# Optimization experiments

Measured on AMD Instinct MI355X. Metric: run time of the kernel, lower is better.

The kernel has to match this reference:

```python
import jax, jax.numpy as jnp
import numpy as np

B, S = 2, 1024
HIDDEN = 2048
NUM_K, NUM_V = 16, 32
DK, DV = 128, 128
KCONV = 4
EPS = 1e-6
KEY_DIM = NUM_K * DK      # 2048
VAL_DIM = NUM_V * DV      # 4096
RATIO = NUM_V // NUM_K    # 2


def setup_inputs() -> dict:
    key = jax.random.key(0)
    ks = jax.random.split(key, 8)
    sc = lambda k, shape, s=0.02: jax.random.normal(k, shape, jnp.float32) * s
    return {
        "hidden_states": jax.random.normal(ks[0], (B, S, HIDDEN), jnp.float32),
        "W_qkvz": sc(ks[1], (HIDDEN, 2 * KEY_DIM + 2 * VAL_DIM)),
        "W_ba": sc(ks[2], (HIDDEN, 2 * NUM_V)),
        "conv_weight": sc(ks[3], (2 * KEY_DIM + VAL_DIM, KCONV), 0.1),
        "A_log": jnp.log(jax.random.uniform(ks[4], (NUM_V,), jnp.float32, 0.001, 16.0)),
        "dt_bias": jnp.ones((NUM_V,), jnp.float32),
        "norm_weight": jnp.ones((DV,), jnp.float32),
        "W_out": sc(ks[5], (VAL_DIM, HIDDEN)),
    }


def _l2norm(x):
    return x * jax.lax.rsqrt(jnp.sum(x * x, axis=-1, keepdims=True) + 1e-6)


def reference(hidden_states, W_qkvz, W_ba, conv_weight, A_log, dt_bias, norm_weight, W_out):
    Bb, Ss, _ = hidden_states.shape
    # fused in_proj + fix_query_key_value_ordering: per k-head layout [q|k|ratio*v|ratio*z]
    qkvz = (hidden_states @ W_qkvz).reshape(Bb, Ss, NUM_K, 2 * DK + 2 * RATIO * DV)
    q = qkvz[..., :DK]                                        # [B,S,NUM_K,DK]
    k = qkvz[..., DK:2 * DK]
    v = qkvz[..., 2 * DK:2 * DK + RATIO * DV].reshape(Bb, Ss, NUM_V, DV)
    z = qkvz[..., 2 * DK + RATIO * DV:].reshape(Bb, Ss, NUM_V, DV)
    ba = (hidden_states @ W_ba).reshape(Bb, Ss, NUM_K, 2 * RATIO)
    b = ba[..., :RATIO].reshape(Bb, Ss, NUM_V)
    a = ba[..., RATIO:].reshape(Bb, Ss, NUM_V)
    # causal depthwise conv over mixed qkv channels + silu (causal_conv1d)
    mixed = jnp.concatenate(
        [q.reshape(Bb, Ss, -1), k.reshape(Bb, Ss, -1), v.reshape(Bb, Ss, -1)], axis=-1)
    x = jnp.transpose(mixed, (0, 2, 1))                       # [B,C,S]
    x = jnp.pad(x, ((0, 0), (0, 0), (KCONV - 1, 0)))
    conv = jax.lax.conv_general_dilated(
        x, conv_weight[:, None, :], (1,), 'VALID',
        feature_group_count=x.shape[1],
        dimension_numbers=('NCH', 'OIH', 'NCH'))
    mixed = jax.nn.silu(jnp.transpose(conv, (0, 2, 1)))       # [B,S,conv_dim]
    q = mixed[..., :KEY_DIM].reshape(Bb, Ss, NUM_K, DK)
    k = mixed[..., KEY_DIM:2 * KEY_DIM].reshape(Bb, Ss, NUM_K, DK)
    v = mixed[..., 2 * KEY_DIM:].reshape(Bb, Ss, NUM_V, DV)
    # GQA: repeat each k-head to its RATIO consecutive v-heads
    q = jnp.repeat(q, RATIO, axis=2)
    k = jnp.repeat(k, RATIO, axis=2)
    q = _l2norm(q) * (DK ** -0.5)
    k = _l2norm(k)
    # fused_gdn_gating: g = -exp(A_log) * softplus(a + dt_bias); beta = sigmoid(b)
    g = -jnp.exp(A_log) * jax.nn.softplus(a + dt_bias)        # [B,S,H] fp32
    beta = jax.nn.sigmoid(b)
    # recurrent gated delta rule scan; state [B,H,DK,DV]
    def step(state, inp):
        qt, kt, vt, gt, bt = inp
        state = state * jnp.exp(gt)[..., None, None]
        pred = jnp.einsum('bhk,bhkv->bhv', kt, state)
        delta = (vt - pred) * bt[..., None]
        state = state + kt[..., None] * delta[..., None, :]
        out = jnp.einsum('bhk,bhkv->bhv', qt, state)
        return state, out

    xs = (q.transpose(1, 0, 2, 3), k.transpose(1, 0, 2, 3), v.transpose(1, 0, 2, 3),
          g.transpose(1, 0, 2), beta.transpose(1, 0, 2))
    state0 = jnp.zeros((Bb, NUM_V, DK, DV), jnp.float32)
    _, core = jax.lax.scan(step, state0, xs)                  # [S,B,H,DV]
    core = core.transpose(1, 0, 2, 3)
    # RMSNormGated (norm_before_gate=True): rmsnorm(x) * w * silu(z)
    var = jnp.mean(core * core, axis=-1, keepdims=True)
    core = core * jax.lax.rsqrt(var + EPS) * norm_weight * jax.nn.silu(z)
    return core.reshape(Bb, Ss, VAL_DIM) @ W_out              # [B,S,HIDDEN]
```

## Files before the change

### kernel.cpp

```cpp
#include <hip/hip_runtime.h>
#include <stdint.h>

#define B_ 2
#define S_ 1024
#define HID 2048
#define NK 16
#define NV 32
#define DK_ 128
#define DV_ 128
#define QKVZ_N 12288
#define TOK (B_*S_)

typedef unsigned short u16;
typedef __bf16 bf16x8 __attribute__((ext_vector_type(8)));
typedef float f32x4 __attribute__((ext_vector_type(4)));
typedef unsigned short u16x8 __attribute__((ext_vector_type(8)));
typedef unsigned short u16x4 __attribute__((ext_vector_type(4)));

__device__ __forceinline__ float bf2f(u16 u) {
    return __builtin_bit_cast(float, (unsigned)u << 16);
}
__device__ __forceinline__ u16 f2bf(float f) {
    unsigned u = __builtin_bit_cast(unsigned, f);
    u += 0x7fff + ((u >> 16) & 1);
    return (u16)(u >> 16);
}

__device__ __forceinline__ void gl16(const void* g, void* l) {
    __builtin_amdgcn_global_load_lds((const __attribute__((address_space(1))) uint32_t*)g,
                                     (__attribute__((address_space(3))) uint32_t*)l, 16, 0, 0);
}

__device__ __forceinline__ bf16x8 fragld(const u16* base, int row, int col, int rowhw) {
    int idx = row * rowhw + ((((col >> 3) ^ (row & 7))) << 3);
    return __builtin_bit_cast(bf16x8, *(const u16x8*)(base + idx));
}
__device__ __forceinline__ int swzidx(int row, int col, int rowhw) {
    return row * rowhw + (((col >> 3) ^ (row & 7)) << 3) + (col & 7);
}

__global__ void k_cvt_bf16(const float* __restrict__ in, u16* __restrict__ out, int n) {
    int i = (blockIdx.x * blockDim.x + threadIdx.x) * 4;
    if (i >= n) return;
    float4 v = *(const float4*)(in + i);
    u16x4 o = { f2bf(v.x), f2bf(v.y), f2bf(v.z), f2bf(v.w) };
    *(u16x4*)(out + i) = o;
}

__global__ void k_transpose(const float* __restrict__ in, u16* __restrict__ out, int R, int C) {
    __shared__ float tile[32][33];
    int c0 = blockIdx.x * 32, r0 = blockIdx.y * 32;
    int tx = threadIdx.x, ty = threadIdx.y;
#pragma unroll
    for (int i = 0; i < 4; i++)
        tile[ty + i * 8][tx] = in[(size_t)(r0 + ty + i * 8) * C + c0 + tx];
    __syncthreads();
#pragma unroll
    for (int i = 0; i < 4; i++)
        out[(size_t)(c0 + ty + i * 8) * R + r0 + tx] = f2bf(tile[tx][ty + i * 8]);
}

template <int OUT_BF16>
__global__ __launch_bounds__(256) void k_gemm(const u16* __restrict__ A, const u16* __restrict__ Bt,
                                              void* __restrict__ Cv, int K, int ldc) {
    __shared__ u16 As[128 * 32];
    __shared__ u16 Bs[128 * 32];
    int tid = threadIdx.x;
    int bm = blockIdx.y, bn = blockIdx.x;
    int wid = tid >> 6, lane = tid & 63;
    int wm = wid >> 1, wn = wid & 1;
    int l15 = lane & 15, lg = lane >> 4;
    const u16* src0 = (wid >> 1) ? (Bt + (size_t)bn * 128 * K) : (A + (size_t)bm * 128 * K);
    u16* ldsb = (wid >> 1) ? Bs : As;
    int cbase = (wid & 1) * 4;
    int lrow = lane >> 2, lcol = (lane & 3) * 8;
    f32x4 acc[4][4] = {};
    for (int k0 = 0; k0 < K; k0 += 32) {
        if (k0) __syncthreads();
#pragma unroll
        for (int c = 0; c < 4; c++) {
            int ch = cbase + c;
            gl16(src0 + (size_t)(16 * ch + lrow) * K + k0 + lcol, (char*)ldsb + ch * 1024);
        }
        __syncthreads();
        bf16x8 af[4], bf[4];
#pragma unroll
        for (int mi = 0; mi < 4; mi++)
            af[mi] = __builtin_bit_cast(bf16x8, *(const u16x8*)&As[(wm * 64 + mi * 16 + l15) * 32 + lg * 8]);
#pragma unroll
        for (int ni = 0; ni < 4; ni++)
            bf[ni] = __builtin_bit_cast(bf16x8, *(const u16x8*)&Bs[(wn * 64 + ni * 16 + l15) * 32 + lg * 8]);
#pragma unroll
        for (int mi = 0; mi < 4; mi++)
#pragma unroll
            for (int ni = 0; ni < 4; ni++)
                acc[mi][ni] = __builtin_amdgcn_mfma_f32_16x16x32_bf16(af[mi], bf[ni], acc[mi][ni], 0, 0, 0);
    }
#pragma unroll
    for (int mi = 0; mi < 4; mi++) {
        int gr0 = bm * 128 + wm * 64 + mi * 16 + lg * 4;
#pragma unroll
        for (int ni = 0; ni < 4; ni++) {
            int gc = bn * 128 + wn * 64 + ni * 16 + l15;
#pragma unroll
            for (int r = 0; r < 4; r++) {
                if (OUT_BF16)
                    ((u16*)Cv)[(size_t)(gr0 + r) * ldc + gc] = f2bf(acc[mi][ni][r]);
                else
                    ((float*)Cv)[(size_t)(gr0 + r) * ldc + gc] = acc[mi][ni][r];
            }
        }
    }
}

__global__ void k_ba(const float* __restrict__ hid, const float* __restrict__ Wba, float* __restrict__ ba) {
    int token = blockIdx.x;
    int c = threadIdx.x;
    const float* h = hid + (size_t)token * HID;
    const float* w = Wba + c;
    float acc = 0.f;
    for (int k = 0; k < HID; k += 4) {
        float4 hv = *(const float4*)(h + k);
        acc += hv.x * w[(size_t)k * 64] + hv.y * w[(size_t)(k + 1) * 64] +
               hv.z * w[(size_t)(k + 2) * 64] + hv.w * w[(size_t)(k + 3) * 64];
    }
    ba[(size_t)token * 64 + c] = acc;
}

__global__ __launch_bounds__(256) void k_conv(const u16* __restrict__ qkvz, const float* __restrict__ ba,
                                              const float* __restrict__ cw, const float* __restrict__ A_log,
                                              const float* __restrict__ dt_bias, u16* __restrict__ qsb,
                                              u16* __restrict__ ksb, u16* __restrict__ vsb,
                                              float2* __restrict__ gb2) {
    __shared__ float sm[4096];
    int token = blockIdx.x;
    int b = token >> 10;
    int t = token & (S_ - 1);
    int tid = threadIdx.x;
    const u16* row3 = qkvz + (size_t)token * QKVZ_N;
#pragma unroll
    for (int i = 0; i < 32; i++) {
        int c = tid + i * 256;
        int col;
        if (c < 2048) col = (c >> 7) * 768 + (c & 127);
        else if (c < 4096) col = ((c - 2048) >> 7) * 768 + 128 + (c & 127);
        else {
            int cc = c - 4096;
            col = (cc >> 8) * 768 + 256 + ((cc >> 7) & 1) * 128 + (cc & 127);
        }
        float4 w = *(const float4*)(cw + c * 4);
        float x3 = bf2f(row3[col]);
        float x2 = (t >= 1) ? bf2f(row3[col - QKVZ_N]) : 0.f;
        float x1 = (t >= 2) ? bf2f(row3[col - 2 * QKVZ_N]) : 0.f;
        float x0 = (t >= 3) ? bf2f(row3[col - 3 * QKVZ_N]) : 0.f;
        float s = w.x * x0 + w.y * x1 + w.z * x2 + w.w * x3;
        s = s / (1.f + __expf(-s));
        if (c < 4096) sm[c] = s;
        else {
            int cc = c - 4096;
            int hv = cc >> 7, d = cc & 127;
            vsb[((size_t)(b * NV + hv) * S_ + t) * 128 + d] = f2bf(s);
        }
    }
    __syncthreads();
    int grp = tid >> 3, l8 = tid & 7;
    float vals[16];
    float ss = 0.f;
    const float* sp = sm + grp * 128 + l8 * 16;
#pragma unroll
    for (int i = 0; i < 16; i++) { vals[i] = sp[i]; ss += vals[i] * vals[i]; }
    ss += __shfl_xor(ss, 1); ss += __shfl_xor(ss, 2); ss += __shfl_xor(ss, 4);
    float scale = rsqrtf(ss + 1e-6f);
    if (grp < 16) scale *= 0.08838834764831845f;
    u16* op = (grp < 16 ? qsb : ksb) + ((size_t)(b * NK + (grp & 15)) * S_ + t) * 128 + l8 * 16;
    u16x8 o0, o1;
#pragma unroll
    for (int i = 0; i < 8; i++) { o0[i] = f2bf(vals[i] * scale); o1[i] = f2bf(vals[i + 8] * scale); }
    *(u16x8*)(op) = o0;
    *(u16x8*)(op + 8) = o1;
    if (tid < 32) {
        int hv = tid;
        float bval = ba[(size_t)token * 64 + (hv >> 1) * 4 + (hv & 1)];
        float aval = ba[(size_t)token * 64 + (hv >> 1) * 4 + 2 + (hv & 1)];
        float x = aval + dt_bias[hv];
        float sp2 = (x > 20.f) ? x : log1pf(__expf(x));
        float graw = -__expf(A_log[hv]) * sp2;
        float bt = 1.f / (1.f + __expf(-bval));
        gb2[(size_t)(b * NV + hv) * S_ + t] = make_float2(graw, bt);
    }
}


__global__ __launch_bounds__(256) void k_prep(const u16* __restrict__ ksb, const u16* __restrict__ qsb,
                                              const float2* __restrict__ gb2, float* __restrict__ Mbuf,
                                              u16* __restrict__ MqB, u16* __restrict__ KtB,
                                              u16* __restrict__ aQB, float* __restrict__ aCB) {
    __shared__ u16 Kl[64 * 128];
    __shared__ u16 Ql[64 * 128];
    __shared__ float QKKK[64 * 68];
    __shared__ float cum[64], bet[64], aex[64], gl[64];
    int bid = blockIdx.x;
    int chunk = bid & 15, hv = (bid >> 4) & 31, b = bid >> 9;
    int hk = hv >> 1;
    size_t ch = bid;
    int tid = threadIdx.x, wid = tid >> 6, lane = tid & 63;
    int l15 = lane & 15, lg = lane >> 4;
    const u16* kg = ksb + ((size_t)(b * NK + hk) * S_ + chunk * 64) * 128;
    const u16* qg = qsb + ((size_t)(b * NK + hk) * S_ + chunk * 64) * 128;
    for (int c = wid; c < 32; c += 4) {
        const u16* src = (c < 16) ? kg : qg;
        u16* dst = (c < 16) ? Kl : Ql;
        int c1 = c & 15;
        int row = c1 * 4 + (lane >> 4);
        int g = lane & 15;
        gl16(src + row * 128 + ((g ^ (row & 7)) << 3), (char*)dst + c1 * 1024 + lane * 16);
    }
    if (tid < 64) {
        float2 gv = gb2[(size_t)(b * NV + hv) * S_ + chunk * 64 + tid];
        gl[tid] = gv.x; bet[tid] = gv.y;
    }
    __syncthreads();
    if (tid == 0) { float s = 0.f; for (int i = 0; i < 64; i++) { s += gl[i]; cum[i] = s; } }
    __syncthreads();
    if (tid < 64) aex[tid] = __expf(cum[tid]);
    {
        f32x4 qk[4] = {};
#pragma unroll
        for (int kk = 0; kk < 4; kk++) {
            bf16x8 af = fragld(Ql, wid * 16 + l15, kk * 32 + lg * 8, 128);
#pragma unroll
            for (int nt = 0; nt < 4; nt++) {
                bf16x8 bk = fragld(Kl, nt * 16 + l15, kk * 32 + lg * 8, 128);
                qk[nt] = __builtin_amdgcn_mfma_f32_16x16x32_bf16(af, bk, qk[nt], 0, 0, 0);
            }
        }
#pragma unroll
        for (int nt = 0; nt < 4; nt++)
#pragma unroll
            for (int r = 0; r < 4; r++)
                QKKK[(wid * 16 + lg * 4 + r) * 68 + nt * 16 + l15] = qk[nt][r];
    }
    __syncthreads();
    {
        int i = tid >> 2, jc = (tid & 3) * 16;
        u16x8 m0, m1;
#pragma unroll
        for (int jj = 0; jj < 16; jj++) {
            int j = jc + jj;
            float v = (j <= i) ? __expf(cum[i] - cum[j]) * QKKK[i * 68 + j] : 0.f;
            if (jj < 8) m0[jj] = f2bf(v); else m1[jj - 8] = f2bf(v);
        }
        *(u16x8*)(MqB + ch * 4096 + i * 64 + jc) = m0;
        *(u16x8*)(MqB + ch * 4096 + i * 64 + jc + 8) = m1;
    }
    __syncthreads();
    {
        f32x4 kkc[4] = {};
#pragma unroll
        for (int kk = 0; kk < 4; kk++) {
            bf16x8 af = fragld(Kl, wid * 16 + l15, kk * 32 + lg * 8, 128);
#pragma unroll
            for (int nt = 0; nt < 4; nt++) {
                bf16x8 bk = fragld(Kl, nt * 16 + l15, kk * 32 + lg * 8, 128);
                kkc[nt] = __builtin_amdgcn_mfma_f32_16x16x32_bf16(af, bk, kkc[nt], 0, 0, 0);
            }
        }
        __syncthreads();
#pragma unroll
        for (int nt = 0; nt < 4; nt++)
#pragma unroll
            for (int r = 0; r < 4; r++)
                QKKK[(wid * 16 + lg * 4 + r) * 68 + nt * 16 + l15] = kkc[nt][r];
    }
    __syncthreads();
    {
        int i = tid >> 2, jc = (tid & 3) * 16;
        float4 out4;
#pragma unroll
        for (int q4 = 0; q4 < 4; q4++) {
#pragma unroll
            for (int e = 0; e < 4; e++) {
                int j = jc + q4 * 4 + e;
                float v = (j < i) ? bet[i] * __expf(cum[i] - cum[j]) * QKKK[i * 68 + j] : 0.f;
                ((float*)&out4)[e] = v;
            }
            *(float4*)(Mbuf + ch * 4096 + i * 64 + jc + q4 * 4) = out4;
        }
    }
    {
        int dk = tid >> 1, jc = (tid & 1) * 32;
#pragma unroll
        for (int q8 = 0; q8 < 4; q8++) {
            u16x8 o;
#pragma unroll
            for (int e = 0; e < 8; e++) {
                int j = jc + q8 * 8 + e;
                o[e] = f2bf(__expf(cum[63] - cum[j]) * bf2f(Kl[swzidx(j, dk, 128)]));
            }
            *(u16x8*)(KtB + ch * 8192 + dk * 64 + jc + q8 * 8) = o;
        }
    }
    {
        int i = tid >> 2, dc = (tid & 3) * 32;
        float a = aex[i];
#pragma unroll
        for (int q8 = 0; q8 < 4; q8++) {
            u16x8 o;
#pragma unroll
            for (int e = 0; e < 8; e++)
                o[e] = f2bf(a * bf2f(Ql[swzidx(i, dc + q8 * 8 + e, 128)]));
            *(u16x8*)(aQB + ch * 8192 + i * 128 + dc + q8 * 8) = o;
        }
    }
    if (tid == 0) aCB[ch] = aex[63];
}

__global__ __launch_bounds__(256) void k_solve(const u16* __restrict__ ksb, const u16* __restrict__ vsb,
                                               const float2* __restrict__ gb2, const float* __restrict__ Mbuf,
                                               float* __restrict__ TvB, u16* __restrict__ WB) {
    __shared__ float Ml[64 * 64];
    __shared__ u16 Kl[64 * 128];
    __shared__ u16 Vl[64 * 128];
    __shared__ u16 bounce[64 * 136];
    __shared__ float cum[64], bet[64], aex[64], gl[64];
    int bid = blockIdx.x;
    int chunk = bid & 15, hv = (bid >> 4) & 31, b = bid >> 9;
    int hk = hv >> 1;
    size_t ch = bid;
    int tid = threadIdx.x, wid = tid >> 6, lane = tid & 63;
    const u16* kg = ksb + ((size_t)(b * NK + hk) * S_ + chunk * 64) * 128;
    const u16* vg = vsb + ((size_t)(b * NV + hv) * S_ + chunk * 64) * 128;
    const float* mg = Mbuf + ch * 4096;
    for (int c = wid; c < 48; c += 4) {
        if (c < 16) gl16((const char*)mg + c * 1024 + lane * 16, (char*)Ml + c * 1024 + lane * 16);
        else if (c < 32) gl16((const char*)kg + (c - 16) * 1024 + lane * 16, (char*)Kl + (c - 16) * 1024 + lane * 16);
        else gl16((const char*)vg + (c - 32) * 1024 + lane * 16, (char*)Vl + (c - 32) * 1024 + lane * 16);
    }
    if (tid < 64) {
        float2 gv = gb2[(size_t)(b * NV + hv) * S_ + chunk * 64 + tid];
        gl[tid] = gv.x; bet[tid] = gv.y;
    }
    __syncthreads();
    if (tid == 0) { float s = 0.f; for (int i = 0; i < 64; i++) { s += gl[i]; cum[i] = s; } }
    __syncthreads();
    if (tid < 64) aex[tid] = __expf(cum[tid]);
    __syncthreads();
    int c = tid;
    float X[64];
    if (c < 128) {
#pragma unroll
        for (int i = 0; i < 64; i++) X[i] = bet[i] * bf2f(Vl[i * 128 + c]);
    } else {
        int d = c - 128;
#pragma unroll
        for (int i = 0; i < 64; i++) X[i] = -bet[i] * aex[i] * bf2f(Kl[i * 128 + d]);
    }
#pragma unroll
    for (int IB = 0; IB < 8; ++IB) {
#pragma unroll
        for (int JB = 0; JB < IB; ++JB) {
#pragma unroll
            for (int ii = 0; ii < 8; ++ii) {
                const float* mr = &Ml[(IB * 8 + ii) * 64 + JB * 8];
                float4 a = *(const float4*)mr, bq = *(const float4*)(mr + 4);
                float x = X[IB * 8 + ii];
                x = fmaf(-a.x, X[JB * 8 + 0], x); x = fmaf(-a.y, X[JB * 8 + 1], x);
                x = fmaf(-a.z, X[JB * 8 + 2], x); x = fmaf(-a.w, X[JB * 8 + 3], x);
                x = fmaf(-bq.x, X[JB * 8 + 4], x); x = fmaf(-bq.y, X[JB * 8 + 5], x);
                x = fmaf(-bq.z, X[JB * 8 + 6], x); x = fmaf(-bq.w, X[JB * 8 + 7], x);
                X[IB * 8 + ii] = x;
            }
        }
#pragma unroll
        for (int ii = 1; ii < 8; ++ii) {
            float x = X[IB * 8 + ii];
#pragma unroll
            for (int jj = 0; jj < ii; ++jj)
                x = fmaf(-Ml[(IB * 8 + ii) * 64 + IB * 8 + jj], X[IB * 8 + jj], x);
            X[IB * 8 + ii] = x;
        }
    }
    if (c < 128) {
        float* o = TvB + ch * 8192 + (size_t)c * 64;
#pragma unroll
        for (int q4 = 0; q4 < 16; q4++) {
            float4 v4 = { X[q4 * 4], X[q4 * 4 + 1], X[q4 * 4 + 2], X[q4 * 4 + 3] };
            *(float4*)(o + q4 * 4) = v4;
        }
    } else {
        int d = c - 128;
#pragma unroll
        for (int i = 0; i < 64; i++) bounce[i * 136 + d] = f2bf(X[i]);
    }
    __syncthreads();
    {
        int i = tid >> 2, dc = (tid & 3) * 32;
#pragma unroll
        for (int q8 = 0; q8 < 4; q8++) {
            u16x8 o;
#pragma unroll
            for (int e = 0; e < 8; e++) o[e] = bounce[i * 136 + dc + q8 * 8 + e];
            *(u16x8*)(WB + ch * 8192 + i * 128 + dc + q8 * 8) = o;
        }
    }
}

__global__ __launch_bounds__(256) void k_chunk(const float* __restrict__ TvB, const u16* __restrict__ WB,
                                               const u16* __restrict__ aQB, const u16* __restrict__ MqB,
                                               const u16* __restrict__ KtB, const float* __restrict__ aCB,
                                               float* __restrict__ core) {
    __shared__ u16 S0h[64 * 128], S0l[64 * 128];
    __shared__ u16 DTh[64 * 64], DTl[64 * 64];
    __shared__ float Tvl[64 * 64];
    __shared__ u16 Wl[64 * 128], aQl[64 * 128];
    __shared__ u16 Mql[64 * 64];
    __shared__ u16 Ktl[128 * 64];
    int bid = blockIdx.x;
    int split = bid & 1, bh = bid >> 1;
    int tid = threadIdx.x, wid = tid >> 6, lane = tid & 63;
    int l15 = lane & 15, lg = lane >> 4;
    float4 z4 = {0.f, 0.f, 0.f, 0.f};
    for (int i = tid; i < 64 * 128 / 8; i += 256) {
        *(float4*)(S0h + i * 8) = z4;
        *(float4*)(S0l + i * 8) = z4;
    }
    for (int chunk = 0; chunk < 16; ++chunk) {
        size_t ch = (size_t)bh * 16 + chunk;
        const char* tvg = (const char*)(TvB + ch * 8192 + (size_t)split * 64 * 64);
        const char* wg = (const char*)(WB + ch * 8192);
        const char* qg = (const char*)(aQB + ch * 8192);
        const char* mg = (const char*)(MqB + ch * 4096);
        const char* kg = (const char*)(KtB + ch * 8192);
        for (int c = wid; c < 72; c += 4) {
            if (c < 16) {
                gl16(tvg + c * 1024 + lane * 16, (char*)Tvl + c * 1024 + lane * 16);
            } else if (c < 32) {
                int cc = c - 16; int row = cc * 4 + (lane >> 4); int g = lane & 15;
                gl16(wg + row * 256 + ((g ^ (row & 7)) << 4), (char*)Wl + cc * 1024 + lane * 16);
            } else if (c < 48) {
                int cc = c - 32; int row = cc * 4 + (lane >> 4); int g = lane & 15;
                gl16(qg + row * 256 + ((g ^ (row & 7)) << 4), (char*)aQl + cc * 1024 + lane * 16);
            } else if (c < 56) {
                int cc = c - 48; int row = cc * 8 + (lane >> 3); int g = lane & 7;
                gl16(mg + row * 128 + ((g ^ (row & 7)) << 4), (char*)Mql + cc * 1024 + lane * 16);
            } else {
                int cc = c - 56; int row = cc * 8 + (lane >> 3); int g = lane & 7;
                gl16(kg + row * 128 + ((g ^ (row & 7)) << 4), (char*)Ktl + cc * 1024 + lane * 16);
            }
        }
        float aC = aCB[ch];
        __syncthreads();
        f32x4 Dacc[4], Oacc[4] = {};
#pragma unroll
        for (int nt = 0; nt < 4; nt++)
#pragma unroll
            for (int r = 0; r < 4; r++)
                Dacc[nt][r] = Tvl[(wid * 16 + lg * 4 + r) * 64 + nt * 16 + l15];
#pragma unroll
        for (int kk = 0; kk < 4; kk++) {
            bf16x8 aH = fragld(S0h, wid * 16 + l15, kk * 32 + lg * 8, 128);
            bf16x8 aL = fragld(S0l, wid * 16 + l15, kk * 32 + lg * 8, 128);
#pragma unroll
            for (int nt = 0; nt < 4; nt++) {
                bf16x8 bW = fragld(Wl, nt * 16 + l15, kk * 32 + lg * 8, 128);
                Dacc[nt] = __builtin_amdgcn_mfma_f32_16x16x32_bf16(aH, bW,
                           __builtin_amdgcn_mfma_f32_16x16x32_bf16(aL, bW, Dacc[nt], 0, 0, 0), 0, 0, 0);
                bf16x8 bQ = fragld(aQl, nt * 16 + l15, kk * 32 + lg * 8, 128);
                Oacc[nt] = __builtin_amdgcn_mfma_f32_16x16x32_bf16(aH, bQ,
                           __builtin_amdgcn_mfma_f32_16x16x32_bf16(aL, bQ, Oacc[nt], 0, 0, 0), 0, 0, 0);
            }
        }
#pragma unroll
        for (int nt = 0; nt < 4; nt++)
#pragma unroll
            for (int r = 0; r < 4; r++) {
                int dv = wid * 16 + lg * 4 + r, t = nt * 16 + l15;
                float x = Dacc[nt][r];
                u16 h = f2bf(x);
                int idx = swzidx(dv, t, 64);
                DTh[idx] = h; DTl[idx] = f2bf(x - bf2f(h));
            }
#pragma unroll
        for (int kk2 = 0; kk2 < 2; kk2++) {
            bf16x8 aDh = fragld(DTh, wid * 16 + l15, kk2 * 32 + lg * 8, 64);
            bf16x8 aDl = fragld(DTl, wid * 16 + l15, kk2 * 32 + lg * 8, 64);
#pragma unroll
            for (int nt = 0; nt < 4; nt++) {
                bf16x8 bM = fragld(Mql, nt * 16 + l15, kk2 * 32 + lg * 8, 64);
                Oacc[nt] = __builtin_amdgcn_mfma_f32_16x16x32_bf16(aDh, bM,
                           __builtin_amdgcn_mfma_f32_16x16x32_bf16(aDl, bM, Oacc[nt], 0, 0, 0), 0, 0, 0);
            }
        }
#pragma unroll
        for (int nt = 0; nt < 4; nt++) {
            float4 o = { Oacc[nt][0], Oacc[nt][1], Oacc[nt][2], Oacc[nt][3] };
            size_t t = (size_t)chunk * 64 + nt * 16 + l15;
            *(float4*)(core + ((size_t)bh * S_ + t) * 128 + split * 64 + wid * 16 + lg * 4) = o;
        }
        f32x4 Sacc[8] = {};
#pragma unroll
        for (int kk2 = 0; kk2 < 2; kk2++) {
            bf16x8 aDh = fragld(DTh, wid * 16 + l15, kk2 * 32 + lg * 8, 64);
            bf16x8 aDl = fragld(DTl, wid * 16 + l15, kk2 * 32 + lg * 8, 64);
#pragma unroll
            for (int nd = 0; nd < 8; nd++) {
                bf16x8 bK = fragld(Ktl, nd * 16 + l15, kk2 * 32 + lg * 8, 64);
                Sacc[nd] = __builtin_amdgcn_mfma_f32_16x16x32_bf16(aDh, bK,
                           __builtin_amdgcn_mfma_f32_16x16x32_bf16(aDl, bK, Sacc[nd], 0, 0, 0), 0, 0, 0);
            }
        }
#pragma unroll
        for (int nd = 0; nd < 8; nd++)
#pragma unroll
            for (int r = 0; r < 4; r++) {
                int dv = wid * 16 + lg * 4 + r, dk = nd * 16 + l15;
                int idx = swzidx(dv, dk, 128);
                float old = bf2f(S0h[idx]) + bf2f(S0l[idx]);
                float nu = fmaf(aC, old, Sacc[nd][r]);
                u16 h = f2bf(nu);
                S0h[idx] = h; S0l[idx] = f2bf(nu - bf2f(h));
            }
        __syncthreads();
    }
}

__global__ __launch_bounds__(256) void k_gate(const float* __restrict__ core, const u16* __restrict__ qkvz,
                                              const float* __restrict__ nw, u16* __restrict__ gated) {
    int token = blockIdx.x, tid = threadIdx.x;
    int b = token >> 10, t = token & (S_ - 1);
    int grp = tid >> 3, l8 = tid & 7;
    const float* cp = core + ((size_t)(b * NV + grp) * S_ + t) * DV_ + l8 * 16;
    float vals[16];
    float ss = 0.f;
#pragma unroll
    for (int i = 0; i < 16; i++) { vals[i] = cp[i]; ss += vals[i] * vals[i]; }
    ss += __shfl_xor(ss, 1); ss += __shfl_xor(ss, 2); ss += __shfl_xor(ss, 4);
    float rms = rsqrtf(ss * (1.0f / DV_) + 1e-6f);
    const u16* zp = qkvz + (size_t)token * QKVZ_N + (grp >> 1) * 768 + 512 + (grp & 1) * 128 + l8 * 16;
    u16* op = gated + ((size_t)token * NV + grp) * DV_ + l8 * 16;
#pragma unroll
    for (int i = 0; i < 16; i++) {
        float z = bf2f(zp[i]);
        float sz = z / (1.f + __expf(-z));
        op[i] = f2bf(vals[i] * rms * nw[l8 * 16 + i] * sz);
    }
}

extern "C" void kernel_launch(void* const* d_in, const int* in_sizes, int n_in,
                              void* d_out, int out_size, void* d_ws, size_t ws_size,
                              hipStream_t stream) {
    const float* hidden = (const float*)d_in[0];
    const float* Wqkvz = (const float*)d_in[1];
    const float* Wba = (const float*)d_in[2];
    const float* convw = (const float*)d_in[3];
    const float* A_log = (const float*)d_in[4];
    const float* dt_bias = (const float*)d_in[5];
    const float* norm_w = (const float*)d_in[6];
    const float* Wout = (const float*)d_in[7];

    char* ws = (char*)d_ws;
    size_t off = 0;
    auto alloc = [&](size_t bytes) -> void* {
        void* p = ws + off;
        off += (bytes + 255) & ~(size_t)255;
        return p;
    };
    u16* hiddenB = (u16*)alloc((size_t)TOK * HID * 2);
    u16* WqT = (u16*)alloc((size_t)QKVZ_N * HID * 2);
    u16* WoT = (u16*)alloc((size_t)HID * 4096 * 2);
    u16* qkvz = (u16*)alloc((size_t)TOK * QKVZ_N * 2);
    float* ba = (float*)alloc((size_t)TOK * 64 * 4);
    u16* qsb = (u16*)alloc((size_t)B_ * NK * S_ * 128 * 2);
    u16* ksb = (u16*)alloc((size_t)B_ * NK * S_ * 128 * 2);
    u16* vsb = (u16*)alloc((size_t)B_ * NV * S_ * 128 * 2);
    float2* gb2 = (float2*)alloc((size_t)B_ * NV * S_ * 8);
    float* Mbuf = (float*)alloc((size_t)1024 * 4096 * 4);
    u16* MqB = (u16*)alloc((size_t)1024 * 4096 * 2);
    u16* KtB = (u16*)alloc((size_t)1024 * 8192 * 2);
    u16* aQB = (u16*)alloc((size_t)1024 * 8192 * 2);
    float* TvB = (float*)alloc((size_t)1024 * 8192 * 4);
    u16* WB = (u16*)alloc((size_t)1024 * 8192 * 2);
    float* aCB = (float*)alloc((size_t)1024 * 4);
    float* core = (float*)alloc((size_t)B_ * NV * S_ * 128 * 4);
    u16* gated = (u16*)alloc((size_t)TOK * 4096 * 2);

    k_cvt_bf16<<<4096, 256, 0, stream>>>(hidden, hiddenB, TOK * HID);
    k_transpose<<<dim3(QKVZ_N / 32, HID / 32), dim3(32, 8), 0, stream>>>(Wqkvz, WqT, HID, QKVZ_N);
    k_transpose<<<dim3(HID / 32, 4096 / 32), dim3(32, 8), 0, stream>>>(Wout, WoT, 4096, HID);
    k_gemm<1><<<dim3(QKVZ_N / 128, TOK / 128), 256, 0, stream>>>(hiddenB, WqT, qkvz, HID, QKVZ_N);
    k_ba<<<TOK, 64, 0, stream>>>(hidden, Wba, ba);
    k_conv<<<TOK, 256, 0, stream>>>(qkvz, ba, convw, A_log, dt_bias, qsb, ksb, vsb, gb2);
    k_prep<<<1024, 256, 0, stream>>>(ksb, qsb, gb2, Mbuf, MqB, KtB, aQB, aCB);
    k_solve<<<1024, 256, 0, stream>>>(ksb, vsb, gb2, Mbuf, TvB, WB);
    k_chunk<<<128, 256, 0, stream>>>(TvB, WB, aQB, MqB, KtB, aCB, core);
    k_gate<<<TOK, 256, 0, stream>>>(core, qkvz, norm_w, gated);
    k_gemm<0><<<dim3(HID / 128, TOK / 128), 256, 0, stream>>>(gated, WoT, d_out, 4096, HID);
}
```

Baseline: 572.4 us.

## Use 256x256 tiled triple-buffered GEMM for the QKVZ input projection

```diff
diff --git a/kernel.cpp b/kernel.cpp
--- a/kernel.cpp
+++ b/kernel.cpp
@@ -58,6 +58,75 @@
 #pragma unroll
     for (int i = 0; i < 4; i++)
         out[(size_t)(c0 + ty + i * 8) * R + r0 + tx] = f2bf(tile[tx][ty + i * 8]);
+}
+
+__global__ __launch_bounds__(512) void k_gemm256(const u16* __restrict__ A, const u16* __restrict__ Bt,
+                                                 u16* __restrict__ C, int K, int ldc) {
+    __shared__ u16 lds[3 * 16384];
+    int tid = threadIdx.x, wid = tid >> 6, lane = tid & 63;
+    int wm = wid >> 2, wn = wid & 3;
+    int l15 = lane & 15, lg = lane >> 4;
+    int bm = blockIdx.y, bn = blockIdx.x;
+    const u16* Ag = A + (size_t)bm * 256 * K;
+    const u16* Bg = Bt + (size_t)bn * 256 * K;
+
+    auto stage = [&](int t, int b) {
+        u16* basebuf = &lds[b * 16384];
+        int kcol = t * 32;
+#pragma unroll
+        for (int j = 0; j < 2; j++) {
+            int chunk = wid * 2 + j;
+            int row = chunk * 16 + (lane >> 2);
+            int gg = ((lane & 3) + 4 - ((row >> 1) & 3)) & 3;
+            gl16(Ag + (size_t)row * K + kcol + gg * 8, (char*)basebuf + chunk * 1024);
+            gl16(Bg + (size_t)row * K + kcol + gg * 8, (char*)(basebuf + 8192) + chunk * 1024);
+        }
+    };
+    auto ldfA = [&](int bsel, int row) -> bf16x8 {
+        const u16* p = &lds[bsel * 16384];
+        int g = (lg + (row >> 1)) & 3;
+        return __builtin_bit_cast(bf16x8, *(const u16x8*)(p + row * 32 + g * 8));
+    };
+    auto ldfB = [&](int bsel, int row) -> bf16x8 {
+        const u16* p = &lds[bsel * 16384 + 8192];
+        int g = (lg + (row >> 1)) & 3;
+        return __builtin_bit_cast(bf16x8, *(const u16x8*)(p + row * 32 + g * 8));
+    };
+
+    f32x4 acc[8][4] = {};
+    int NT = K >> 5;
+    stage(0, 0);
+    stage(1, 1);
+    for (int t = 0; t < NT; ++t) {
+        if (t < NT - 1) asm volatile("s_waitcnt vmcnt(4)" ::: "memory");
+        else            asm volatile("s_waitcnt vmcnt(0)" ::: "memory");
+        __builtin_amdgcn_s_barrier();
+        if (t + 2 < NT) stage(t + 2, (t + 2) % 3);
+        int bsel = t % 3;
+        bf16x8 bfr[4];
+#pragma unroll
+        for (int ni = 0; ni < 4; ni++) bfr[ni] = ldfB(bsel, wn * 64 + ni * 16 + l15);
+        __builtin_amdgcn_s_setprio(1);
+#pragma unroll
+        for (int mi = 0; mi < 8; mi++) {
+            bf16x8 af = ldfA(bsel, wm * 128 + mi * 16 + l15);
+#pragma unroll
+            for (int ni = 0; ni < 4; ni++)
+                acc[mi][ni] = __builtin_amdgcn_mfma_f32_16x16x32_bf16(af, bfr[ni], acc[mi][ni], 0, 0, 0);
+        }
+        __builtin_amdgcn_s_setprio(0);
+    }
+#pragma unroll
+    for (int mi = 0; mi < 8; mi++) {
+        int gr0 = bm * 256 + wm * 128 + mi * 16 + lg * 4;
+#pragma unroll
+        for (int ni = 0; ni < 4; ni++) {
+            int gc = bn * 256 + wn * 64 + ni * 16 + l15;
+#pragma unroll
+            for (int r = 0; r < 4; r++)
+                C[(size_t)(gr0 + r) * ldc + gc] = f2bf(acc[mi][ni][r]);
+        }
+    }
 }
 
 template <int OUT_BF16>
@@ -587,7 +656,7 @@
     k_cvt_bf16<<<4096, 256, 0, stream>>>(hidden, hiddenB, TOK * HID);
     k_transpose<<<dim3(QKVZ_N / 32, HID / 32), dim3(32, 8), 0, stream>>>(Wqkvz, WqT, HID, QKVZ_N);
     k_transpose<<<dim3(HID / 32, 4096 / 32), dim3(32, 8), 0, stream>>>(Wout, WoT, 4096, HID);
-    k_gemm<1><<<dim3(QKVZ_N / 128, TOK / 128), 256, 0, stream>>>(hiddenB, WqT, qkvz, HID, QKVZ_N);
+    k_gemm256<<<dim3(QKVZ_N / 256, TOK / 256), 512, 0, stream>>>(hiddenB, WqT, qkvz, HID, QKVZ_N);
     k_ba<<<TOK, 64, 0, stream>>>(hidden, Wba, ba);
     k_conv<<<TOK, 256, 0, stream>>>(qkvz, ba, convw, A_log, dt_bias, qsb, ksb, vsb, gb2);
     k_prep<<<1024, 256, 0, stream>>>(ksb, qsb, gb2, Mbuf, MqB, KtB, aQB, aCB);
```

Measured after the change: 583.0 us. About the same (+1.8%).
